# Kernel optimization log

Hardware: AMD Instinct MI355X
Metric: run time of the kernel (lower is better)

The kernel has to match this reference:

```python
import jax, jax.numpy as jnp
import numpy as np

B, S, D = 2, 1024, 1024
C, HID, H = 32, 64, 16  # compress_dim, prg_hidden_dim, num_heads


def setup_inputs() -> dict:
    key = jax.random.key(0)
    ks = jax.random.split(key, 7)
    def glorot(k, shape):
        lim = 1.0 / np.sqrt(shape[0])
        return jax.random.uniform(k, shape, jnp.float32, -lim, lim)
    return {
        "x": jax.random.normal(ks[0], (B, S, D), jnp.float32),
        "Wc": glorot(ks[1], (D, C)),
        "bc": jnp.zeros((C,), jnp.float32),
        "W1": glorot(ks[2], (2 * C, HID)),
        "b1": jnp.zeros((HID,), jnp.float32),
        "W2": glorot(ks[3], (HID, H)),
        "b2": jnp.zeros((H,), jnp.float32),
    }


def reference(x, Wc, bc, W1, b1, W2, b2):
    Bc, Sc, _ = x.shape
    # compress: [B,S,C]
    xc = x @ Wc + bc
    # pairwise concat via broadcast (same values as tile+concat)
    token_i = jnp.broadcast_to(xc[:, :, None, :], (Bc, Sc, Sc, C))
    token_j = jnp.broadcast_to(xc[:, None, :, :], (Bc, Sc, Sc, C))
    pair_emb = jnp.concatenate([token_i, token_j], axis=-1)  # [B,S,S,2C]
    h = jax.nn.gelu(pair_emb @ W1 + b1)                      # [B,S,S,HID]
    prg_bias = h @ W2 + b2                                   # [B,S,S,H]
    return jnp.transpose(prg_bias, (0, 3, 1, 2))             # [B,H,S,S]
```

## Files before the change

kernel.cpp:

```cpp
#include <hip/hip_runtime.h>
#include <hip/hip_fp16.h>

#define SDIM 1024

typedef _Float16 f16;
typedef _Float16 f16x2v __attribute__((ext_vector_type(2)));
typedef _Float16 f16x8 __attribute__((ext_vector_type(8)));
typedef __attribute__((ext_vector_type(4))) float f32x4;

union FragH { unsigned int u[4]; f16x8 f; uint4 q; };
union H2U  { unsigned int u; __half2 h; f16x2v v; };

__device__ __forceinline__ unsigned int addgelu_pair(unsigned int au, unsigned int bu) {
    const __half2 kC5  = __float2half2_rn(-0.006912f);
    const __half2 kC4  = __float2half2_rn( 0.019336f);
    const __half2 kC3  = __float2half2_rn(-0.040316f);
    const __half2 kC2  = __float2half2_rn( 0.090220f);
    const __half2 kC1  = __float2half2_rn(-0.185452f);
    const __half2 kC0  = __float2half2_rn( 0.455649f);
    const __half2 kXA  = __float2half2_rn( 0.2222222f);
    const __half2 kXB  = __float2half2_rn(-1.0f);
    const __half2 kHalf= __float2half2_rn( 0.5f);
    const f16x2v vHi = { (f16)3.0f, (f16)3.0f };
    const f16x2v vLo = { (f16)-3.0f, (f16)-3.0f };
    H2U A, B, T, C, G;
    A.u = au; B.u = bu;
    __half2 t  = __hadd2(A.h, B.h);
    T.h = t;
    C.v = __builtin_elementwise_min(__builtin_elementwise_max(T.v, vLo), vHi);
    __half2 tc = C.h;
    __half2 s  = __hmul2(tc, tc);
    __half2 x  = __hfma2(s, kXA, kXB);
    __half2 w  = __hfma2(kC5, x, kC4);
    w = __hfma2(w, x, kC3);
    w = __hfma2(w, x, kC2);
    w = __hfma2(w, x, kC1);
    w = __hfma2(w, x, kC0);
    __half2 m  = __hmul2(tc, w);
    __half2 sg = __hfma2(m, kHalf, kHalf);
    G.h = __hmul2(t, sg);
    return G.u;
}

__global__ __launch_bounds__(256) void compute_uv(
    const float* __restrict__ x, const float* __restrict__ Wc,
    const float* __restrict__ bc, const float* __restrict__ W1,
    const float* __restrict__ b1, const float* __restrict__ W2,
    f16* __restrict__ u, f16* __restrict__ v, f16* __restrict__ W2h)
{
    __shared__ float xrow[4 * 1024];
    __shared__ float part[4 * 8 * 32];
    __shared__ float xc[4 * 32];
    const int tid = threadIdx.x;
    const size_t bs0 = (size_t)blockIdx.x * 4;

    if (blockIdx.x == 0) {
        #pragma unroll
        for (int e = 0; e < 4; ++e) {
            const int flat = tid * 4 + e;
            const int h = flat >> 6, k = flat & 63;
            W2h[flat] = (f16)W2[k * 16 + h];
        }
    }

    const float4* xin = (const float4*)(x + bs0 * 1024);
    #pragma unroll
    for (int it = 0; it < 4; ++it)
        ((float4*)xrow)[it * 256 + tid] = xin[it * 256 + tid];
    __syncthreads();
    {
        const int c = tid & 31, p = tid >> 5;
        float acc[4] = {0.f, 0.f, 0.f, 0.f};
        #pragma unroll 4
        for (int dd = 0; dd < 128; ++dd) {
            const int d = p * 128 + dd;
            const float wv = Wc[d * 32 + c];
            #pragma unroll
            for (int r = 0; r < 4; ++r)
                acc[r] = __builtin_fmaf(xrow[r * 1024 + d], wv, acc[r]);
        }
        #pragma unroll
        for (int r = 0; r < 4; ++r)
            part[r * 256 + p * 32 + c] = acc[r];
    }
    __syncthreads();
    if (tid < 128) {
        const int r = tid >> 5, c = tid & 31;
        float s = bc[c];
        #pragma unroll
        for (int p = 0; p < 8; ++p) s += part[r * 256 + p * 32 + c];
        xc[r * 32 + c] = s;
    }
    __syncthreads();
    {
        const int h = tid & 63;
        const int rr = tid >> 6;
        float ua = b1[h], va = 0.0f;
        #pragma unroll
        for (int cc = 0; cc < 32; ++cc) {
            const float xv = xc[rr * 32 + cc];
            ua = __builtin_fmaf(xv, W1[cc * 64 + h], ua);
            va = __builtin_fmaf(xv, W1[(32 + cc) * 64 + h], va);
        }
        u[(bs0 + rr) * 64 + h] = (f16)ua;
        v[(bs0 + rr) * 64 + h] = (f16)va;
    }
}

__global__ __launch_bounds__(256, 6) void prg_main(
    const f16* __restrict__ u, const f16* __restrict__ v,
    const f16* __restrict__ W2h, const float* __restrict__ b2,
    float* __restrict__ out)
{
    const int tid  = threadIdx.x;
    const int lane = tid & 63;
    const int w    = tid >> 6;
    const int jb   = blockIdx.x * 32;
    const int ib   = blockIdx.y * 32;
    const int b    = blockIdx.z;

    __shared__ f16 u_lds[32][64];

    {
        const int row = tid >> 3;
        const int col = (tid & 7) * 8;
        *(uint4*)&u_lds[row][col] =
            *(const uint4*)(u + ((size_t)(b * SDIM + ib + row) * 64 + col));
    }

    const int lg = lane >> 4;
    const int lr = lane & 15;
    const int k0 = lg * 8;
    const int jw = jb + (w & 1) * 16;
    const int iw = (w >> 1) * 16;

    const f16* vp = v + ((size_t)(b * SDIM + jw + lr) * 64);
    const uint4 vlo = *(const uint4*)(vp + k0);
    const uint4 vhi = *(const uint4*)(vp + k0 + 32);

    FragH w2lo, w2hi;
    w2lo.q = *(const uint4*)(W2h + lr * 64 + k0);
    w2hi.q = *(const uint4*)(W2h + lr * 64 + k0 + 32);

    const float b2h = b2[lr];

    __syncthreads();

    float* ob = out + ((size_t)(b * 16 + lr) * SDIM + (ib + iw)) * SDIM + jw + lg * 4;

    #pragma unroll
    for (int g = 0; g < 4; ++g) {
        f32x4 acc[4];
        #pragma unroll
        for (int q = 0; q < 4; ++q) {
            const int il = iw + g * 4 + q;
            const uint4 alo = *(const uint4*)&u_lds[il][k0];
            const uint4 ahi = *(const uint4*)&u_lds[il][k0 + 32];
            FragH glo, ghi;
            glo.u[0] = addgelu_pair(alo.x, vlo.x);
            glo.u[1] = addgelu_pair(alo.y, vlo.y);
            glo.u[2] = addgelu_pair(alo.z, vlo.z);
            glo.u[3] = addgelu_pair(alo.w, vlo.w);
            ghi.u[0] = addgelu_pair(ahi.x, vhi.x);
            ghi.u[1] = addgelu_pair(ahi.y, vhi.y);
            ghi.u[2] = addgelu_pair(ahi.z, vhi.z);
            ghi.u[3] = addgelu_pair(ahi.w, vhi.w);
            f32x4 a = {b2h, b2h, b2h, b2h};
            a = __builtin_amdgcn_mfma_f32_16x16x32_f16(glo.f, w2lo.f, a, 0, 0, 0);
            a = __builtin_amdgcn_mfma_f32_16x16x32_f16(ghi.f, w2hi.f, a, 0, 0, 0);
            acc[q] = a;
        }
        #pragma unroll
        for (int q = 0; q < 4; ++q)
            *(float4*)(ob + (size_t)(g * 4 + q) * SDIM) = *(float4*)&acc[q];
    }
}

extern "C" void kernel_launch(void* const* d_in, const int* in_sizes, int n_in,
                              void* d_out, int out_size, void* d_ws, size_t ws_size,
                              hipStream_t stream) {
    const float* x  = (const float*)d_in[0];
    const float* Wc = (const float*)d_in[1];
    const float* bc = (const float*)d_in[2];
    const float* W1 = (const float*)d_in[3];
    const float* b1 = (const float*)d_in[4];
    const float* W2 = (const float*)d_in[5];
    const float* b2 = (const float*)d_in[6];
    float* out = (float*)d_out;

    f16* u   = (f16*)d_ws;
    f16* v   = u + 2 * SDIM * 64;
    f16* W2h = v + 2 * SDIM * 64;

    compute_uv<<<dim3(512), dim3(256), 0, stream>>>(x, Wc, bc, W1, b1, W2, u, v, W2h);
    prg_main<<<dim3(32, 32, 2), dim3(256), 0, stream>>>(u, v, W2h, b2, out);
}
```

Baseline: 49.76 us.

## Compute GELU in fp32, pipeline stores with compute, drop occupancy hint

```diff
diff --git a/kernel.cpp b/kernel.cpp
--- a/kernel.cpp
+++ b/kernel.cpp
@@ -4,42 +4,35 @@
 #define SDIM 1024
 
 typedef _Float16 f16;
-typedef _Float16 f16x2v __attribute__((ext_vector_type(2)));
 typedef _Float16 f16x8 __attribute__((ext_vector_type(8)));
+typedef __fp16 fp16x2 __attribute__((ext_vector_type(2)));
 typedef __attribute__((ext_vector_type(4))) float f32x4;
 
 union FragH { unsigned int u[4]; f16x8 f; uint4 q; };
-union H2U  { unsigned int u; __half2 h; f16x2v v; };
+
+__device__ __forceinline__ float gelu_core(float t) {
+    float tc = __builtin_amdgcn_fmed3f(t, -3.0f, 3.0f);
+    float s  = tc * tc;
+    float x  = __builtin_fmaf(s, 0.2222222f, -1.0f);
+    float w  = __builtin_fmaf(-0.003456f, x, 0.009668f);
+    w = __builtin_fmaf(w, x, -0.020158f);
+    w = __builtin_fmaf(w, x,  0.045110f);
+    w = __builtin_fmaf(w, x, -0.092726f);
+    w = __builtin_fmaf(w, x,  0.2278245f);
+    float sg = __builtin_fmaf(tc, w, 0.5f);
+    return t * sg;
+}
 
 __device__ __forceinline__ unsigned int addgelu_pair(unsigned int au, unsigned int bu) {
-    const __half2 kC5  = __float2half2_rn(-0.006912f);
-    const __half2 kC4  = __float2half2_rn( 0.019336f);
-    const __half2 kC3  = __float2half2_rn(-0.040316f);
-    const __half2 kC2  = __float2half2_rn( 0.090220f);
-    const __half2 kC1  = __float2half2_rn(-0.185452f);
-    const __half2 kC0  = __float2half2_rn( 0.455649f);
-    const __half2 kXA  = __float2half2_rn( 0.2222222f);
-    const __half2 kXB  = __float2half2_rn(-1.0f);
-    const __half2 kHalf= __float2half2_rn( 0.5f);
-    const f16x2v vHi = { (f16)3.0f, (f16)3.0f };
-    const f16x2v vLo = { (f16)-3.0f, (f16)-3.0f };
-    H2U A, B, T, C, G;
+    union { unsigned int u; __half2 h; } A, B, T;
     A.u = au; B.u = bu;
-    __half2 t  = __hadd2(A.h, B.h);
-    T.h = t;
-    C.v = __builtin_elementwise_min(__builtin_elementwise_max(T.v, vLo), vHi);
-    __half2 tc = C.h;
-    __half2 s  = __hmul2(tc, tc);
-    __half2 x  = __hfma2(s, kXA, kXB);
-    __half2 w  = __hfma2(kC5, x, kC4);
-    w = __hfma2(w, x, kC3);
-    w = __hfma2(w, x, kC2);
-    w = __hfma2(w, x, kC1);
-    w = __hfma2(w, x, kC0);
-    __half2 m  = __hmul2(tc, w);
-    __half2 sg = __hfma2(m, kHalf, kHalf);
-    G.h = __hmul2(t, sg);
-    return G.u;
+    T.h = __hadd2(A.h, B.h);
+    const float tl = (float)__builtin_bit_cast(f16, (unsigned short)(T.u & 0xFFFFu));
+    const float th = (float)__builtin_bit_cast(f16, (unsigned short)(T.u >> 16));
+    const float gl = gelu_core(tl);
+    const float gh = gelu_core(th);
+    fp16x2 p = __builtin_amdgcn_cvt_pkrtz(gl, gh);
+    return __builtin_bit_cast(unsigned int, p);
 }
 
 __global__ __launch_bounds__(256) void compute_uv(
@@ -62,7 +55,6 @@
             W2h[flat] = (f16)W2[k * 16 + h];
         }
     }
-
     const float4* xin = (const float4*)(x + bs0 * 1024);
     #pragma unroll
     for (int it = 0; it < 4; ++it)
@@ -107,7 +99,7 @@
     }
 }
 
-__global__ __launch_bounds__(256, 6) void prg_main(
+__global__ __launch_bounds__(256) void prg_main(
     const f16* __restrict__ u, const f16* __restrict__ v,
     const f16* __restrict__ W2h, const float* __restrict__ b2,
     float* __restrict__ out)
@@ -148,32 +140,40 @@
 
     float* ob = out + ((size_t)(b * 16 + lr) * SDIM + (ib + iw)) * SDIM + jw + lg * 4;
 
+#define GM(IL, ACC)                                                               \
+    {                                                                             \
+        const uint4 alo = *(const uint4*)&u_lds[IL][k0];                          \
+        const uint4 ahi = *(const uint4*)&u_lds[IL][k0 + 32];                     \
+        FragH glo, ghi;                                                           \
+        glo.u[0] = addgelu_pair(alo.x, vlo.x);                                    \
+        glo.u[1] = addgelu_pair(alo.y, vlo.y);                                    \
+        glo.u[2] = addgelu_pair(alo.z, vlo.z);                                    \
+        glo.u[3] = addgelu_pair(alo.w, vlo.w);                                    \
+        ghi.u[0] = addgelu_pair(ahi.x, vhi.x);                                    \
+        ghi.u[1] = addgelu_pair(ahi.y, vhi.y);                                    \
+        ghi.u[2] = addgelu_pair(ahi.z, vhi.z);                                    \
+        ghi.u[3] = addgelu_pair(ahi.w, vhi.w);                                    \
+        f32x4 a_ = {b2h, b2h, b2h, b2h};                                          \
+        a_ = __builtin_amdgcn_mfma_f32_16x16x32_f16(glo.f, w2lo.f, a_, 0, 0, 0);  \
+        a_ = __builtin_amdgcn_mfma_f32_16x16x32_f16(ghi.f, w2hi.f, a_, 0, 0, 0);  \
+        ACC = a_;                                                                 \
+    }
+#define ST(IL, ACC) *(float4*)(ob + (size_t)(IL) * SDIM) = *(float4*)&(ACC);
+
+    f32x4 accA, accB;
+    GM(iw + 0, accA)
     #pragma unroll
-    for (int g = 0; g < 4; ++g) {
-        f32x4 acc[4];
-        #pragma unroll
-        for (int q = 0; q < 4; ++q) {
-            const int il = iw + g * 4 + q;
-            const uint4 alo = *(const uint4*)&u_lds[il][k0];
-            const uint4 ahi = *(const uint4*)&u_lds[il][k0 + 32];
-            FragH glo, ghi;
-            glo.u[0] = addgelu_pair(alo.x, vlo.x);
-            glo.u[1] = addgelu_pair(alo.y, vlo.y);
-            glo.u[2] = addgelu_pair(alo.z, vlo.z);
-            glo.u[3] = addgelu_pair(alo.w, vlo.w);
-            ghi.u[0] = addgelu_pair(ahi.x, vhi.x);
-            ghi.u[1] = addgelu_pair(ahi.y, vhi.y);
-            ghi.u[2] = addgelu_pair(ahi.z, vhi.z);
-            ghi.u[3] = addgelu_pair(ahi.w, vhi.w);
-            f32x4 a = {b2h, b2h, b2h, b2h};
-            a = __builtin_amdgcn_mfma_f32_16x16x32_f16(glo.f, w2lo.f, a, 0, 0, 0);
-            a = __builtin_amdgcn_mfma_f32_16x16x32_f16(ghi.f, w2hi.f, a, 0, 0, 0);
-            acc[q] = a;
-        }
-        #pragma unroll
-        for (int q = 0; q < 4; ++q)
-            *(float4*)(ob + (size_t)(g * 4 + q) * SDIM) = *(float4*)&acc[q];
+    for (int p = 0; p < 7; ++p) {
+        GM(iw + 2 * p + 1, accB)
+        ST(2 * p, accA)
+        GM(iw + 2 * p + 2, accA)
+        ST(2 * p + 1, accB)
     }
+    GM(iw + 15, accB)
+    ST(14, accA)
+    ST(15, accB)
+#undef GM
+#undef ST
 }
 
 extern "C" void kernel_launch(void* const* d_in, const int* in_sizes, int n_in,
```

After: 58.25 us. +17.1%, slower.
